# Optimization experiments

Measured on AMD Instinct MI355X. Metric: run time of the kernel, lower is better.

Reference implementation:

```python
import jax, jax.numpy as jnp
import numpy as np

B, S, D = 4, 2048, 1024
NH = 16
HD = D // NH

def setup_inputs() -> dict:
    key = jax.random.key(0)
    ks = jax.random.split(key, 5)
    s = 1.0 / np.sqrt(D)
    x = jax.random.normal(ks[0], (B, S, D), dtype=jnp.float32)
    Wq = jax.random.uniform(ks[1], (D, D), jnp.float32, -s, s)
    Wk = jax.random.uniform(ks[2], (D, D), jnp.float32, -s, s)
    Wv = jax.random.uniform(ks[3], (D, D), jnp.float32, -s, s)
    Wo = jax.random.uniform(ks[4], (D, D), jnp.float32, -s, s)
    return {"x": x, "Wq": Wq, "Wk": Wk, "Wv": Wv, "Wo": Wo}

def reference(x, Wq, Wk, Wv, Wo):
    # x: [B, S, D]; W*: [D_in, D_out] stored as (out,in) torch-style -> apply x @ W.T
    def proj_heads(W):
        t = jnp.einsum('bsd,ed->bse', x, W)              # [B,S,D]
        return t.reshape(B, S, NH, HD).transpose(0, 2, 1, 3)  # [B,NH,S,HD]
    q = proj_heads(Wq)
    k = proj_heads(Wk)
    v = proj_heads(Wv)
    scale = 1.0 / jnp.sqrt(jnp.asarray(HD, dtype=x.dtype))
    scores = jnp.einsum('bhqd,bhkd->bhqk', q, k) * scale   # [B,NH,S,S]
    attn = jax.nn.softmax(scores, axis=-1)
    y = jnp.einsum('bhqk,bhkd->bhqd', attn, v)             # [B,NH,S,HD]
    y = y.transpose(0, 2, 1, 3).reshape(B, S, D)
    y = jnp.einsum('bsd,ed->bse', y, Wo)                   # out_proj, no bias
    return y
```

## Files before the change

kernel.cpp:

```cpp
#include <hip/hip_runtime.h>
#include <hip/hip_bf16.h>
#include <math.h>

#define B_  4
#define S_  2048
#define D_  1024
#define NH_ 16
#define HD_ 64

typedef __attribute__((ext_vector_type(8))) short bf16x8;
typedef __attribute__((ext_vector_type(4))) float f32x4;
typedef __attribute__((ext_vector_type(4))) uint  u32x4;

#define VMCNT(n)  asm volatile("s_waitcnt vmcnt(" #n ")" ::: "memory")
#define LGKMCNT0  asm volatile("s_waitcnt lgkmcnt(0)" ::: "memory")
#define SCHEDB()  __builtin_amdgcn_sched_barrier(0)
#define BARRIER() __builtin_amdgcn_s_barrier()

__device__ inline ushort f2bf(float f) {
    uint u = __builtin_bit_cast(uint, f);
    uint r = (u + 0x7fffu + ((u >> 16) & 1u)) >> 16;
    return (ushort)r;
}

__device__ inline uint cvt_pk_bf16(float lo, float hi) {
    uint r;
    asm volatile("v_cvt_pk_bf16_f32 %0, %1, %2" : "=v"(r) : "v"(lo), "v"(hi));
    return r;
}

__device__ inline float exp2_raw(float x) {
    float r;
    asm volatile("v_exp_f32 %0, %1" : "=v"(r) : "v"(x));
    return r;
}

__global__ __launch_bounds__(256) void cast_all(const float* __restrict__ x,
                                                const float* __restrict__ w0,
                                                const float* __restrict__ w1,
                                                const float* __restrict__ w2,
                                                const float* __restrict__ w3,
                                                ushort* __restrict__ xb,
                                                ushort* __restrict__ wb,
                                                int nx, int nw) {
    int i = (blockIdx.x * 256 + threadIdx.x) * 4;
    const float* src;
    ushort* dst;
    if (i < nx) {
        src = x + i;
        dst = xb + i;
    } else {
        int j = i - nx;
        int t = j >> 20;
        int off = j & (nw - 1);
        src = (t == 0 ? w0 : t == 1 ? w1 : t == 2 ? w2 : w3) + off;
        dst = wb + (size_t)t * nw + off;
    }
    float4 f = *reinterpret_cast<const float4*>(src);
    ushort4 o = {f2bf(f.x), f2bf(f.y), f2bf(f.z), f2bf(f.w)};
    *reinterpret_cast<ushort4*>(dst) = o;
}

template <int MODE>
__global__ __launch_bounds__(256) void gemm128(const ushort* __restrict__ A,
                                               const ushort* __restrict__ W,
                                               void* __restrict__ Cv,
                                               int M, int Nw, int K) {
    __shared__ ushort As[2][128 * 32];
    __shared__ ushort Ws[2][128 * 32];
    const int tid = threadIdx.x;

    const int gx = gridDim.x;
    const int nwg = gx * gridDim.y;
    const int f = blockIdx.y * gx + blockIdx.x;
    const int cpx = nwg >> 3;
    const int tileid = (f & 7) * cpx + (f >> 3);
    const int m0 = (tileid / gx) * 128;
    const int n0 = (tileid % gx) * 128;

    const int lane = tid & 63;
    const int w = tid >> 6;
    const int wr = (w >> 1) * 64;
    const int wc = (w & 1) * 64;
    const int fr = lane & 15;
    const int fq = lane >> 4;

    f32x4 acc[4][4] = {};

    auto STAGE = [&](int k0, int bb) {
#pragma unroll
        for (int it = 0; it < 2; ++it) {
            int c = tid + it * 256;
            int row = c >> 2;
            int col = (c & 3) * 8;
            const ushort* ga = &A[(size_t)(m0 + row) * K + k0 + col];
            const ushort* gw = &W[(size_t)(n0 + row) * K + k0 + col];
            __builtin_amdgcn_global_load_lds(
                (const __attribute__((address_space(1))) uint32_t*)((const void*)ga),
                (__attribute__((address_space(3))) uint32_t*)((void*)&As[bb][c * 8]), 16, 0, 0);
            __builtin_amdgcn_global_load_lds(
                (const __attribute__((address_space(1))) uint32_t*)((const void*)gw),
                (__attribute__((address_space(3))) uint32_t*)((void*)&Ws[bb][c * 8]), 16, 0, 0);
        }
    };
    auto COMPUTE = [&](int bb) {
        bf16x8 af[4], bfv[4];
#pragma unroll
        for (int m = 0; m < 4; ++m)
            af[m] = *reinterpret_cast<const bf16x8*>(&As[bb][(wr + m * 16 + fr) * 32 + fq * 8]);
#pragma unroll
        for (int n = 0; n < 4; ++n)
            bfv[n] = *reinterpret_cast<const bf16x8*>(&Ws[bb][(wc + n * 16 + fr) * 32 + fq * 8]);
        __builtin_amdgcn_s_setprio(1);
#pragma unroll
        for (int m = 0; m < 4; ++m)
#pragma unroll
            for (int n = 0; n < 4; ++n)
                acc[m][n] = __builtin_amdgcn_mfma_f32_16x16x32_bf16(af[m], bfv[n], acc[m][n], 0, 0, 0);
        __builtin_amdgcn_s_setprio(0);
    };

    const int NK = K >> 5;
    STAGE(0, 0);
    VMCNT(0);
    BARRIER(); SCHEDB();
    for (int t = 0; t < NK - 1; ++t) {
        const int cur = t & 1;
        STAGE((t + 1) * 32, cur ^ 1);
        SCHEDB();
        COMPUTE(cur);
        VMCNT(0);
        BARRIER(); SCHEDB();
    }
    COMPUTE((NK - 1) & 1);

    if (MODE == 0) {
        const int tensor = n0 >> 10;
        ushort* C = (ushort*)Cv + (size_t)tensor * ((size_t)M * 1024);
        const float sc = (tensor == 0) ? 0.18033688011112042f : 1.0f;
        const int nb = n0 & 1023;
#pragma unroll
        for (int m = 0; m < 4; ++m)
#pragma unroll
            for (int n = 0; n < 4; ++n) {
                int col = nb + wc + n * 16 + fr;
                int rowb = m0 + wr + m * 16 + fq * 4;
#pragma unroll
                for (int r = 0; r < 4; ++r)
                    C[(size_t)(rowb + r) * 1024 + col] = f2bf(acc[m][n][r] * sc);
            }
    } else {
        float* C = (float*)Cv;
#pragma unroll
        for (int m = 0; m < 4; ++m)
#pragma unroll
            for (int n = 0; n < 4; ++n) {
                int col = n0 + wc + n * 16 + fr;
                int rowb = m0 + wr + m * 16 + fq * 4;
#pragma unroll
                for (int r = 0; r < 4; ++r)
                    C[(size_t)(rowb + r) * Nw + col] = acc[m][n][r];
            }
    }
}

__global__ __launch_bounds__(256, 4) void attn_mfma(const ushort* __restrict__ Qg,
                                                    const ushort* __restrict__ Kg,
                                                    const ushort* __restrict__ Vg,
                                                    ushort* __restrict__ Yg) {
    __shared__ ushort SH[2 * 8192];

    const int tid = threadIdx.x;
    const int lane = tid & 63;
    const int w = tid >> 6;
    const int fr = lane & 15;
    const int fq = lane >> 4;

    const int lin = blockIdx.x;
    const int qt = (lin >> 3) & 15;
    const int bh = (lin & 7) * 8 + (lin >> 7);
    const int b = bh >> 4;
    const int h = bh & 15;
    const size_t hbase = (size_t)b * (S_ * D_) + (size_t)h * HD_;
    const int NT = S_ / 64;

    bf16x8 qf[2][2];
#pragma unroll
    for (int m = 0; m < 2; ++m)
#pragma unroll
        for (int kk = 0; kk < 2; ++kk)
            qf[m][kk] = *reinterpret_cast<const bf16x8*>(
                &Qg[hbase + (size_t)(qt * 128 + w * 32 + m * 16 + fr) * D_ + kk * 32 + fq * 8]);

    uint rdoff[2][4];
#pragma unroll
    for (int kk = 0; kk < 2; ++kk)
#pragma unroll
        for (int n = 0; n < 4; ++n)
            rdoff[kk][n] = (uint)((n * 16 + fr) * 64 + 8 * (((kk << 2) + fq) ^ (fr & 7)));
    uint vwoff[2];
#pragma unroll
    for (int t = 0; t < 2; ++t)
        vwoff[t] = (uint)(lane * 64 + 8 * (((w << 1) + t) ^ (lane & 7)));

    const int c0i = tid, c1i = tid + 256;
    const int krow0 = c0i >> 3, kslot0 = (c0i & 7) ^ (krow0 & 7);
    const int krow1 = c1i >> 3, kslot1 = (c1i & 7) ^ (krow1 & 7);

    f32x4 oy[2][4] = {};
    f32x4 lacc[2] = {};

    const u32x4 onesu = {0x3F803F80u, 0x3F803F80u, 0x3F803F80u, 0x3F803F80u};
    const bf16x8 onesf = __builtin_bit_cast(bf16x8, onesu);

    uint vpk[8];

    auto STAGEK = [&](int kt, int bb) {
        const ushort* g0 = &Kg[hbase + (size_t)(kt * 64 + krow0) * D_ + kslot0 * 8];
        const ushort* g1 = &Kg[hbase + (size_t)(kt * 64 + krow1) * D_ + kslot1 * 8];
        __builtin_amdgcn_global_load_lds(
            (const __attribute__((address_space(1))) uint32_t*)((const void*)g0),
            (__attribute__((address_space(3))) uint32_t*)((void*)&SH[bb + c0i * 8]), 16, 0, 0);
        __builtin_amdgcn_global_load_lds(
            (const __attribute__((address_space(1))) uint32_t*)((const void*)g1),
            (__attribute__((address_space(3))) uint32_t*)((void*)&SH[bb + c1i * 8]), 16, 0, 0);
    };
    auto VLOAD = [&](int kt) {
        const ushort* vp = &Vg[hbase + (size_t)(kt * 64) * D_ + lane];
#pragma unroll
        for (int jj = 0; jj < 8; ++jj) {
            int c = w * 16 + jj * 2;
            int key = (c & 32) + ((c >> 3) & 3) * 4 + (c & 3) + ((c >> 2) & 1) * 16;
            uint lo = vp[(size_t)key * D_];
            uint hi = vp[(size_t)(key + 1) * D_];
            vpk[jj] = lo | (hi << 16);
        }
    };
    auto VWRITE = [&](int bb) {
#pragma unroll
        for (int t = 0; t < 2; ++t) {
            u32x4 a = {vpk[t * 4 + 0], vpk[t * 4 + 1], vpk[t * 4 + 2], vpk[t * 4 + 3]};
            *reinterpret_cast<bf16x8*>(&SH[bb + 4096 + vwoff[t]]) =
                __builtin_bit_cast(bf16x8, a);
        }
    };
    auto QKT = [&](f32x4 (&sc)[2][4], int bb) {
#pragma unroll
        for (int m = 0; m < 2; ++m)
#pragma unroll
            for (int n = 0; n < 4; ++n) sc[m][n] = f32x4{0.f, 0.f, 0.f, 0.f};
        __builtin_amdgcn_s_setprio(1);
#pragma unroll
        for (int kk = 0; kk < 2; ++kk)
#pragma unroll
            for (int n = 0; n < 4; ++n) {
                bf16x8 kf = *reinterpret_cast<const bf16x8*>(&SH[bb + rdoff[kk][n]]);
                sc[0][n] = __builtin_amdgcn_mfma_f32_16x16x32_bf16(kf, qf[0][kk], sc[0][n], 0, 0, 0);
                sc[1][n] = __builtin_amdgcn_mfma_f32_16x16x32_bf16(kf, qf[1][kk], sc[1][n], 0, 0, 0);
            }
        __builtin_amdgcn_s_setprio(0);
    };
    auto SMPV = [&](f32x4 (&sc)[2][4], int bb) {
        uint pk[2][4][2];
#pragma unroll
        for (int m = 0; m < 2; ++m) {
#pragma unroll
            for (int n = 0; n < 4; ++n)
#pragma unroll
                for (int r = 0; r < 4; ++r)
                    sc[m][n][r] = exp2_raw(sc[m][n][r]);
#pragma unroll
            for (int n = 0; n < 4; ++n) {
                pk[m][n][0] = cvt_pk_bf16(sc[m][n][0], sc[m][n][1]);
                pk[m][n][1] = cvt_pk_bf16(sc[m][n][2], sc[m][n][3]);
            }
        }
        __builtin_amdgcn_s_setprio(1);
#pragma unroll
        for (int kk = 0; kk < 2; ++kk) {
            u32x4 a0 = {pk[0][2 * kk][0], pk[0][2 * kk][1], pk[0][2 * kk + 1][0], pk[0][2 * kk + 1][1]};
            u32x4 a1 = {pk[1][2 * kk][0], pk[1][2 * kk][1], pk[1][2 * kk + 1][0], pk[1][2 * kk + 1][1]};
            bf16x8 pf0 = __builtin_bit_cast(bf16x8, a0);
            bf16x8 pf1 = __builtin_bit_cast(bf16x8, a1);
            lacc[0] = __builtin_amdgcn_mfma_f32_16x16x32_bf16(pf0, onesf, lacc[0], 0, 0, 0);
            lacc[1] = __builtin_amdgcn_mfma_f32_16x16x32_bf16(pf1, onesf, lacc[1], 0, 0, 0);
#pragma unroll
            for (int n = 0; n < 4; ++n) {
                bf16x8 vf = *reinterpret_cast<const bf16x8*>(&SH[bb + 4096 + rdoff[kk][n]]);
                oy[0][n] = __builtin_amdgcn_mfma_f32_16x16x32_bf16(pf0, vf, oy[0][n], 0, 0, 0);
                oy[1][n] = __builtin_amdgcn_mfma_f32_16x16x32_bf16(pf1, vf, oy[1][n], 0, 0, 0);
            }
        }
        __builtin_amdgcn_s_setprio(0);
    };

    VLOAD(0);
    VWRITE(0);
    STAGEK(0, 0);
    SCHEDB();
    VLOAD(1);
    VMCNT(16);
    LGKMCNT0;
    BARRIER();
    SCHEDB();

    f32x4 sc[2][4];
    for (int t = 0; t < NT - 2; ++t) {
        const int A = (t & 1) * 8192, Bb = 8192 - A;
        STAGEK(t + 1, Bb);
        SCHEDB();
        QKT(sc, A);
        VWRITE(Bb);
        VLOAD(t + 2);
        SMPV(sc, A);
        VMCNT(16);
        LGKMCNT0;
        BARRIER();
        SCHEDB();
    }
    {
        const int A = ((NT - 2) & 1) * 8192, Bb = 8192 - A;
        STAGEK(NT - 1, Bb);
        SCHEDB();
        QKT(sc, A);
        VWRITE(Bb);
        SMPV(sc, A);
        VMCNT(0);
        LGKMCNT0;
        BARRIER();
        SCHEDB();
    }
    {
        const int A = ((NT - 1) & 1) * 8192;
        QKT(sc, A);
        SMPV(sc, A);
    }

#pragma unroll
    for (int m = 0; m < 2; ++m) {
#pragma unroll
        for (int r = 0; r < 4; ++r) {
            float inv = 1.0f / lacc[m][r];
            int row = qt * 128 + w * 32 + m * 16 + fq * 4 + r;
#pragma unroll
            for (int n = 0; n < 4; ++n)
                Yg[hbase + (size_t)row * D_ + n * 16 + fr] = f2bf(oy[m][n][r] * inv);
        }
    }
}

extern "C" void kernel_launch(void* const* d_in, const int* in_sizes, int n_in,
                              void* d_out, int out_size, void* d_ws, size_t ws_size,
                              hipStream_t stream) {
    const float* x  = (const float*)d_in[0];
    const float* Wq = (const float*)d_in[1];
    const float* Wk = (const float*)d_in[2];
    const float* Wv = (const float*)d_in[3];
    const float* Wo = (const float*)d_in[4];
    float* out = (float*)d_out;

    const size_t nx = (size_t)B_ * S_ * D_;
    const size_t nw = (size_t)D_ * D_;

    ushort* xb = (ushort*)d_ws;
    ushort* wb = xb + nx;
    ushort* qb = wb + 4 * nw;
    ushort* kb = qb + nx;
    ushort* vb = kb + nx;
    ushort* yb = vb + nx;

    dim3 blk(256);
    const int ncast = (int)((nx + 4 * nw) / 4 / 256);
    hipLaunchKernelGGL(cast_all, dim3(ncast), blk, 0, stream,
                       x, Wq, Wk, Wv, Wo, xb, wb, (int)nx, (int)nw);

    const int M = B_ * S_;
    dim3 gqkv(3072 / 128, M / 128);
    hipLaunchKernelGGL((gemm128<0>), gqkv, blk, 0, stream, xb, wb, qb, M, 3072, D_);

    dim3 gattn(1024);
    hipLaunchKernelGGL(attn_mfma, gattn, blk, 0, stream, qb, kb, vb, yb);

    dim3 gproj(D_ / 128, M / 128);
    hipLaunchKernelGGL((gemm128<1>), gproj, blk, 0, stream, yb, wb + 3 * nw, out, M, D_, D_);
}
```

Before: 187.2 us.

## Write V pre-transposed from QKV GEMM and triple-buffer GEMM K loop

The QKV GEMM epilogue now writes V in a per-head transposed, key-permuted layout, so the attention kernel can stage V into LDS with async global-to-LDS loads like K. This removes the register-based strided V gather and LDS write from the attention inner loop. Separately, the GEMM moves from double to triple-buffered LDS staging with a prefetch distance of two tiles. Costs: the V epilogue stores are scattered (short strided writes), GEMM LDS use grows, and attention now waits on vmcnt(0) every iteration.

```diff
diff --git a/kernel.cpp b/kernel.cpp
--- a/kernel.cpp
+++ b/kernel.cpp
@@ -13,7 +13,6 @@
 typedef __attribute__((ext_vector_type(4))) uint  u32x4;
 
 #define VMCNT(n)  asm volatile("s_waitcnt vmcnt(" #n ")" ::: "memory")
-#define LGKMCNT0  asm volatile("s_waitcnt lgkmcnt(0)" ::: "memory")
 #define SCHEDB()  __builtin_amdgcn_sched_barrier(0)
 #define BARRIER() __builtin_amdgcn_s_barrier()
 
@@ -34,6 +33,11 @@
     asm volatile("v_exp_f32 %0, %1" : "=v"(r) : "v"(x));
     return r;
 }
+
+#define GLOAD_LDS(gp, lp) \
+    __builtin_amdgcn_global_load_lds( \
+        (const __attribute__((address_space(1))) uint32_t*)((const void*)(gp)), \
+        (__attribute__((address_space(3))) uint32_t*)((void*)(lp)), 16, 0, 0)
 
 __global__ __launch_bounds__(256) void cast_all(const float* __restrict__ x,
                                                 const float* __restrict__ w0,
@@ -66,8 +70,7 @@
                                                const ushort* __restrict__ W,
                                                void* __restrict__ Cv,
                                                int M, int Nw, int K) {
-    __shared__ ushort As[2][128 * 32];
-    __shared__ ushort Ws[2][128 * 32];
+    __shared__ ushort SH[3 * 8192];
     const int tid = threadIdx.x;
 
     const int gx = gridDim.x;
@@ -93,24 +96,18 @@
             int c = tid + it * 256;
             int row = c >> 2;
             int col = (c & 3) * 8;
-            const ushort* ga = &A[(size_t)(m0 + row) * K + k0 + col];
-            const ushort* gw = &W[(size_t)(n0 + row) * K + k0 + col];
-            __builtin_amdgcn_global_load_lds(
-                (const __attribute__((address_space(1))) uint32_t*)((const void*)ga),
-                (__attribute__((address_space(3))) uint32_t*)((void*)&As[bb][c * 8]), 16, 0, 0);
-            __builtin_amdgcn_global_load_lds(
-                (const __attribute__((address_space(1))) uint32_t*)((const void*)gw),
-                (__attribute__((address_space(3))) uint32_t*)((void*)&Ws[bb][c * 8]), 16, 0, 0);
+            GLOAD_LDS(&A[(size_t)(m0 + row) * K + k0 + col], &SH[bb + c * 8]);
+            GLOAD_LDS(&W[(size_t)(n0 + row) * K + k0 + col], &SH[bb + 4096 + c * 8]);
         }
     };
     auto COMPUTE = [&](int bb) {
         bf16x8 af[4], bfv[4];
 #pragma unroll
         for (int m = 0; m < 4; ++m)
-            af[m] = *reinterpret_cast<const bf16x8*>(&As[bb][(wr + m * 16 + fr) * 32 + fq * 8]);
+            af[m] = *reinterpret_cast<const bf16x8*>(&SH[bb + (wr + m * 16 + fr) * 32 + fq * 8]);
 #pragma unroll
         for (int n = 0; n < 4; ++n)
-            bfv[n] = *reinterpret_cast<const bf16x8*>(&Ws[bb][(wc + n * 16 + fr) * 32 + fq * 8]);
+            bfv[n] = *reinterpret_cast<const bf16x8*>(&SH[bb + 4096 + (wc + n * 16 + fr) * 32 + fq * 8]);
         __builtin_amdgcn_s_setprio(1);
 #pragma unroll
         for (int m = 0; m < 4; ++m)
@@ -122,33 +119,57 @@
 
     const int NK = K >> 5;
     STAGE(0, 0);
-    VMCNT(0);
+    STAGE(32, 8192);
+    VMCNT(4);
     BARRIER(); SCHEDB();
-    for (int t = 0; t < NK - 1; ++t) {
-        const int cur = t & 1;
-        STAGE((t + 1) * 32, cur ^ 1);
-        SCHEDB();
-        COMPUTE(cur);
-        VMCNT(0);
-        BARRIER(); SCHEDB();
-    }
-    COMPUTE((NK - 1) & 1);
+
+    int ba = 0, bbuf = 8192, bc = 16384;
+    for (int t = 0; t < NK; ++t) {
+        if (t + 2 < NK) { STAGE((t + 2) * 32, bc); SCHEDB(); }
+        COMPUTE(ba);
+        if (t + 1 < NK) {
+            if (t + 2 < NK) { VMCNT(4); } else { VMCNT(0); }
+            BARRIER(); SCHEDB();
+        }
+        int tmp = ba; ba = bbuf; bbuf = bc; bc = tmp;
+    }
 
     if (MODE == 0) {
         const int tensor = n0 >> 10;
         ushort* C = (ushort*)Cv + (size_t)tensor * ((size_t)M * 1024);
         const float sc = (tensor == 0) ? 0.18033688011112042f : 1.0f;
         const int nb = n0 & 1023;
-#pragma unroll
-        for (int m = 0; m < 4; ++m)
-#pragma unroll
-            for (int n = 0; n < 4; ++n) {
-                int col = nb + wc + n * 16 + fr;
-                int rowb = m0 + wr + m * 16 + fq * 4;
-#pragma unroll
-                for (int r = 0; r < 4; ++r)
-                    C[(size_t)(rowb + r) * 1024 + col] = f2bf(acc[m][n][r] * sc);
-            }
+        if (tensor == 2) {
+#pragma unroll
+            for (int m = 0; m < 4; ++m)
+#pragma unroll
+                for (int n = 0; n < 4; ++n) {
+                    int colv = nb + wc + n * 16 + fr;
+                    int hh = colv >> 6, dd = colv & 63;
+                    int rowb = m0 + wr + m * 16 + fq * 4;
+                    int bb2 = rowb >> 11;
+                    int s0 = rowb & 2047;
+                    int c = s0 & 63;
+                    int spb = (s0 & ~63) | (32 * (c >> 5) + 8 * ((c >> 2) & 3) +
+                                            4 * ((c >> 4) & 1));
+                    ushort* vt = (ushort*)C;
+                    size_t base = ((size_t)(bb2 * 16 + hh) * 64 + dd) * 2048 + spb;
+#pragma unroll
+                    for (int r = 0; r < 4; ++r)
+                        vt[base + r] = f2bf(acc[m][n][r]);
+                }
+        } else {
+#pragma unroll
+            for (int m = 0; m < 4; ++m)
+#pragma unroll
+                for (int n = 0; n < 4; ++n) {
+                    int col = nb + wc + n * 16 + fr;
+                    int rowb = m0 + wr + m * 16 + fq * 4;
+#pragma unroll
+                    for (int r = 0; r < 4; ++r)
+                        C[(size_t)(rowb + r) * 1024 + col] = f2bf(acc[m][n][r] * sc);
+                }
+        }
     } else {
         float* C = (float*)Cv;
 #pragma unroll
@@ -166,7 +187,7 @@
 
 __global__ __launch_bounds__(256, 4) void attn_mfma(const ushort* __restrict__ Qg,
                                                     const ushort* __restrict__ Kg,
-                                                    const ushort* __restrict__ Vg,
+                                                    const ushort* __restrict__ VtG,
                                                     ushort* __restrict__ Yg) {
     __shared__ ushort SH[2 * 8192];
 
@@ -182,6 +203,7 @@
     const int b = bh >> 4;
     const int h = bh & 15;
     const size_t hbase = (size_t)b * (S_ * D_) + (size_t)h * HD_;
+    const size_t vtbase = (size_t)bh * (64 * 2048);
     const int NT = S_ / 64;
 
     bf16x8 qf[2][2];
@@ -198,14 +220,12 @@
 #pragma unroll
         for (int n = 0; n < 4; ++n)
             rdoff[kk][n] = (uint)((n * 16 + fr) * 64 + 8 * (((kk << 2) + fq) ^ (fr & 7)));
-    uint vwoff[2];
-#pragma unroll
-    for (int t = 0; t < 2; ++t)
-        vwoff[t] = (uint)(lane * 64 + 8 * (((w << 1) + t) ^ (lane & 7)));
 
     const int c0i = tid, c1i = tid + 256;
     const int krow0 = c0i >> 3, kslot0 = (c0i & 7) ^ (krow0 & 7);
     const int krow1 = c1i >> 3, kslot1 = (c1i & 7) ^ (krow1 & 7);
+    const int vd0 = c0i >> 3, vj0 = ((c0i & 7) ^ (vd0 & 7)) * 8;
+    const int vd1 = c1i >> 3, vj1 = ((c1i & 7) ^ (vd1 & 7)) * 8;
 
     f32x4 oy[2][4] = {};
     f32x4 lacc[2] = {};
@@ -213,36 +233,13 @@
     const u32x4 onesu = {0x3F803F80u, 0x3F803F80u, 0x3F803F80u, 0x3F803F80u};
     const bf16x8 onesf = __builtin_bit_cast(bf16x8, onesu);
 
-    uint vpk[8];
-
     auto STAGEK = [&](int kt, int bb) {
-        const ushort* g0 = &Kg[hbase + (size_t)(kt * 64 + krow0) * D_ + kslot0 * 8];
-        const ushort* g1 = &Kg[hbase + (size_t)(kt * 64 + krow1) * D_ + kslot1 * 8];
-        __builtin_amdgcn_global_load_lds(
-            (const __attribute__((address_space(1))) uint32_t*)((const void*)g0),
-            (__attribute__((address_space(3))) uint32_t*)((void*)&SH[bb + c0i * 8]), 16, 0, 0);
-        __builtin_amdgcn_global_load_lds(
-            (const __attribute__((address_space(1))) uint32_t*)((const void*)g1),
-            (__attribute__((address_space(3))) uint32_t*)((void*)&SH[bb + c1i * 8]), 16, 0, 0);
-    };
-    auto VLOAD = [&](int kt) {
-        const ushort* vp = &Vg[hbase + (size_t)(kt * 64) * D_ + lane];
-#pragma unroll
-        for (int jj = 0; jj < 8; ++jj) {
-            int c = w * 16 + jj * 2;
-            int key = (c & 32) + ((c >> 3) & 3) * 4 + (c & 3) + ((c >> 2) & 1) * 16;
-            uint lo = vp[(size_t)key * D_];
-            uint hi = vp[(size_t)(key + 1) * D_];
-            vpk[jj] = lo | (hi << 16);
-        }
-    };
-    auto VWRITE = [&](int bb) {
-#pragma unroll
-        for (int t = 0; t < 2; ++t) {
-            u32x4 a = {vpk[t * 4 + 0], vpk[t * 4 + 1], vpk[t * 4 + 2], vpk[t * 4 + 3]};
-            *reinterpret_cast<bf16x8*>(&SH[bb + 4096 + vwoff[t]]) =
-                __builtin_bit_cast(bf16x8, a);
-        }
+        GLOAD_LDS(&Kg[hbase + (size_t)(kt * 64 + krow0) * D_ + kslot0 * 8], &SH[bb + c0i * 8]);
+        GLOAD_LDS(&Kg[hbase + (size_t)(kt * 64 + krow1) * D_ + kslot1 * 8], &SH[bb + c1i * 8]);
+    };
+    auto STAGEV = [&](int kt, int bb) {
+        GLOAD_LDS(&VtG[vtbase + (size_t)vd0 * 2048 + kt * 64 + vj0], &SH[bb + 4096 + c0i * 8]);
+        GLOAD_LDS(&VtG[vtbase + (size_t)vd1 * 2048 + kt * 64 + vj1], &SH[bb + 4096 + c1i * 8]);
     };
     auto QKT = [&](f32x4 (&sc)[2][4], int bb) {
 #pragma unroll
@@ -294,46 +291,18 @@
         __builtin_amdgcn_s_setprio(0);
     };
 
-    VLOAD(0);
-    VWRITE(0);
     STAGEK(0, 0);
-    SCHEDB();
-    VLOAD(1);
-    VMCNT(16);
-    LGKMCNT0;
-    BARRIER();
-    SCHEDB();
+    STAGEV(0, 0);
+    VMCNT(0);
+    BARRIER(); SCHEDB();
 
     f32x4 sc[2][4];
-    for (int t = 0; t < NT - 2; ++t) {
+    for (int t = 0; t < NT; ++t) {
         const int A = (t & 1) * 8192, Bb = 8192 - A;
-        STAGEK(t + 1, Bb);
-        SCHEDB();
-        QKT(sc, A);
-        VWRITE(Bb);
-        VLOAD(t + 2);
-        SMPV(sc, A);
-        VMCNT(16);
-        LGKMCNT0;
-        BARRIER();
-        SCHEDB();
-    }
-    {
-        const int A = ((NT - 2) & 1) * 8192, Bb = 8192 - A;
-        STAGEK(NT - 1, Bb);
-        SCHEDB();
-        QKT(sc, A);
-        VWRITE(Bb);
-        SMPV(sc, A);
-        VMCNT(0);
-        LGKMCNT0;
-        BARRIER();
-        SCHEDB();
-    }
-    {
-        const int A = ((NT - 1) & 1) * 8192;
+        if (t + 1 < NT) { STAGEK(t + 1, Bb); STAGEV(t + 1, Bb); SCHEDB(); }
         QKT(sc, A);
         SMPV(sc, A);
+        if (t + 1 < NT) { VMCNT(0); BARRIER(); SCHEDB(); }
     }
 
 #pragma unroll
@@ -366,8 +335,8 @@
     ushort* wb = xb + nx;
     ushort* qb = wb + 4 * nw;
     ushort* kb = qb + nx;
-    ushort* vb = kb + nx;
-    ushort* yb = vb + nx;
+    ushort* vt = kb + nx;
+    ushort* yb = vt + nx;
 
     dim3 blk(256);
     const int ncast = (int)((nx + 4 * nw) / 4 / 256);
@@ -379,7 +348,7 @@
     hipLaunchKernelGGL((gemm128<0>), gqkv, blk, 0, stream, xb, wb, qb, M, 3072, D_);
 
     dim3 gattn(1024);
-    hipLaunchKernelGGL(attn_mfma, gattn, blk, 0, stream, qb, kb, vb, yb);
+    hipLaunchKernelGGL(attn_mfma, gattn, blk, 0, stream, qb, kb, vt, yb);
 
     dim3 gproj(D_ / 128, M / 128);
     hipLaunchKernelGGL((gemm128<1>), gproj, blk, 0, stream, yb, wb + 3 * nw, out, M, D_, D_);
```

New measurement: 165.7 us. -11.5%, faster.
